# Performance work log

Hardware: AMD Instinct MI355X
Metric: run time of the kernel (lower is better)

## Reference

```python
import jax, jax.numpy as jnp
import numpy as np

B, N, D = 32, 2048, 128
HALF = D // 2
DT = 0.01  # interval = [0.0, 0.01], euler solver -> single step of size 0.01


def setup_inputs() -> dict:
    key = jax.random.key(0)
    ks = jax.random.split(key, 10)
    x = jax.random.normal(ks[0], (B, N, D), dtype=jnp.float32)
    hz = jax.random.normal(ks[1], (B, N, D), dtype=jnp.float32)
    # row-normalized random adjacency so adj @ h stays O(1) (avoids tanh saturation)
    adj = jax.random.uniform(ks[2], (N, N), dtype=jnp.float32) / N
    W1 = jax.random.normal(ks[3], (D, D), dtype=jnp.float32) * 0.05
    W2 = jax.random.normal(ks[4], (D, D), dtype=jnp.float32) * 0.05
    Wa = jax.random.normal(ks[5], (2 * D, 2 * D), dtype=jnp.float32) * 0.05
    ba = jnp.zeros((2 * D,), dtype=jnp.float32)
    Wb = jax.random.normal(ks[6], (2 * D, D), dtype=jnp.float32) * 0.05
    bb = jnp.zeros((D,), dtype=jnp.float32)
    # nn.Parameter init is zeros in torch; randomize in [0,0.1] for a nontrivial baseline
    eps = jax.random.uniform(ks[7], (B, N, HALF), dtype=jnp.float32) * 0.1
    return {"x": x, "hz": hz, "adj": adj, "W1": W1, "W2": W2,
            "Wa": Wa, "ba": ba, "Wb": Wb, "bb": bb, "eps": eps}


def reference(x, hz, adj, W1, W2, Wa, ba, Wb, bb, eps):
    # MLP gating: Linear(2D,2D) -> ReLU -> Linear(2D,D) -> Tanh
    u = jnp.concatenate([x, hz], axis=-1)            # [B,N,2D]
    h = jnp.tanh(jax.nn.relu(u @ Wa + ba) @ Wb + bb)  # [B,N,D]

    def gnn_func(h, W):
        # f(t, h) = tanh(A @ h @ W)  (graph diffusion ODE func)
        return jnp.tanh(jnp.einsum('nm,bmd->bnd', adj, h) @ W)

    def euler_step(h, W):
        # odeint(euler, t=[0, 0.01]): one step y1 = y0 + dt * f(0, y0)
        return h + DT * gnn_func(h, W)

    eps_c = jnp.clip(eps, 0.0, 0.1)
    for _ in range(2):
        h_f = euler_step(h, W1)[..., :HALF]                      # [B,N,D/2]
        h = jnp.concatenate([h_f, h[..., HALF:]], axis=-1)       # [B,N,D]
        h_s = eps_c * euler_step(h, W2)[..., HALF:]              # [B,N,D/2]
        h = jnp.concatenate([h_f, h_s], axis=-1)                 # [B,N,D]
    return h
```

## Files before the change

### kernel.cpp

```cpp
#include <hip/hip_runtime.h>


typedef unsigned short u16;
typedef unsigned char  u8;
typedef unsigned int   u32;
typedef unsigned long long u64;
typedef __attribute__((ext_vector_type(8))) short bf8;
typedef __attribute__((ext_vector_type(4))) float f4;

#define AS1 __attribute__((address_space(1)))
#define AS3 __attribute__((address_space(3)))

__device__ __forceinline__ void gl_lds16(const void* g, void* l) {
  __builtin_amdgcn_global_load_lds((const AS1 u32*)g, (AS3 u32*)l, 16, 0, 0);
}
__device__ __forceinline__ float bf2f(u16 v) {
  u32 u = ((u32)v) << 16; return __builtin_bit_cast(float, u);
}
__device__ __forceinline__ u16 f2bf(float f) {
  u32 u = __builtin_bit_cast(u32, f);
  return (u16)((u + 0x7fffu + ((u >> 16) & 1u)) >> 16);
}
__device__ __forceinline__ u8 f2fp8(float f) {
  u32 u = __builtin_bit_cast(u32, f);
  u32 s = (u >> 24) & 0x80u;
  int e = (int)((u >> 23) & 0xFFu) - 127;
  u32 m = u & 0x7FFFFFu;
  if (e > 8 || (e == 8 && m >= 0x700000u)) return (u8)(s | 0x7Eu);
  if (e >= -6) {
    u32 keep = m >> 20, rest = m & 0xFFFFFu;
    keep += (rest > 0x80000u || (rest == 0x80000u && (keep & 1u))) ? 1u : 0u;
    u32 v = ((u32)(e + 7) << 3) + keep;
    if (v >= 0x7Fu) v = 0x7Eu;
    return (u8)(s | v);
  }
  if (e < -10) return (u8)s;
  u32 mm = 0x800000u | m;
  int sh = 14 - e;
  u32 q = mm >> sh, rem = mm & ((1u << sh) - 1u), half = 1u << (sh - 1);
  q += (rem > half || (rem == half && (q & 1u))) ? 1u : 0u;
  return (u8)(s | q);
}
__device__ __forceinline__ float ldf(const void* p, size_t i, u32 isf32) {
  return isf32 ? ((const float*)p)[i] : bf2f(((const u16*)p)[i]);
}

__device__ __forceinline__ void stage128x32(const u16* grow0, int stride, u16* lds,
                                            int wave, int lane) {
  int r0 = wave * 16 + (lane >> 2);
  int c0 = (lane & 3) * 8;
  gl_lds16(grow0 + (size_t)r0 * stride + c0, lds + wave * 512);
  gl_lds16(grow0 + (size_t)(64 + r0) * stride + c0, lds + 2048 + wave * 512);
}

__global__ void detect_dtype(const u16* __restrict__ x_raw, u32* __restrict__ flag) {
  __shared__ int s;
  int tid = threadIdx.x;
  if (tid == 0) s = 0;
  __syncthreads();
  int huge = 0;
#pragma unroll
  for (int j = 0; j < 16; ++j) {
    u16 v = x_raw[tid * 16 + j];
    u32 e = (v >> 7) & 0xFF;
    if (e >= 0xC0) huge = 1;
  }
  if (huge) atomicOr(&s, 1);
  __syncthreads();
  if (tid == 0) flag[0] = (u32)s;
}

__global__ void cvt_fp8(const void* __restrict__ in, u8* __restrict__ out,
                        int n, const u32* __restrict__ flag) {
  u32 isf32 = flag[0];
  int gid = blockIdx.x * 256 + threadIdx.x;
  if (gid * 4 >= n) return;
  size_t i = (size_t)gid * 4;
  u32 pk = 0;
#pragma unroll
  for (int j = 0; j < 4; ++j)
    pk |= (u32)f2fp8(ldf(in, i + j, isf32) * 65536.0f) << (8 * j);
  *(u32*)&out[i] = pk;
}

__global__ void prep_weights(const void* __restrict__ Wa, const void* __restrict__ Wb,
                             const void* __restrict__ W1, const void* __restrict__ W2,
                             u16* __restrict__ WaT, u16* __restrict__ WbT,
                             u16* __restrict__ W1T, u16* __restrict__ W2T,
                             const u32* __restrict__ flag) {
  u32 isf32 = flag[0];
  int i = blockIdx.x * 256 + threadIdx.x;
  if (i < 65536) {
    int o = i >> 8, k = i & 255; WaT[o * 256 + k] = f2bf(ldf(Wa, (size_t)k * 256 + o, isf32));
  } else if (i < 98304) {
    int j = i - 65536; int o = j >> 8, k = j & 255;
    WbT[o * 256 + k] = f2bf(ldf(Wb, (size_t)k * 128 + o, isf32));
  } else if (i < 106496) {
    int j = i - 98304; int jj = j >> 7, k = j & 127;
    W1T[jj * 128 + k] = f2bf(ldf(W1, (size_t)k * 128 + jj, isf32));
  } else {
    int j = i - 106496; int jj = j >> 7, k = j & 127;
    W2T[jj * 128 + k] = f2bf(ldf(W2, (size_t)k * 128 + 64 + jj, isf32));
  }
}

__global__ __launch_bounds__(256, 2) void mlp_fused(const void* __restrict__ x,
                                                    const void* __restrict__ hz,
                                                    const u16* __restrict__ WaT,
                                                    const void* __restrict__ ba,
                                                    const u16* __restrict__ WbT,
                                                    const void* __restrict__ bb,
                                                    const u16* __restrict__ W1T,
                                                    u16* __restrict__ hT,
                                                    u8* __restrict__ hW,
                                                    const u32* __restrict__ flag) {
  __shared__ __align__(16) u16 Z[64 * 264];
  __shared__ __align__(16) u16 pool[10240];
  u16* lA = pool;
  u16* lB = pool + 2048;
  u16* hN = pool;
  u32 isf32 = flag[0];
  int tid = threadIdx.x, lane = tid & 63, wave = tid >> 6;
  int col = lane & 15, quad = lane >> 4;
  int r0 = blockIdx.x * 64;
  int b = r0 >> 11;

  f4 acc[4][4] = {};
  for (int kk = 0; kk < 8; ++kk) {
    int k0 = kk * 32;
    const void* src = (kk < 4) ? x : hz;
    int csrc = (kk < 4) ? k0 : (k0 - 128);
    __syncthreads();
    {
      int row = tid >> 2, c0 = (tid & 3) * 8;
      size_t g = (size_t)(r0 + row) * 128 + csrc + c0;
      uint4 pk;
      if (isf32) {
        f4 v0 = *(const f4*)&((const float*)src)[g];
        f4 v1 = *(const f4*)&((const float*)src)[g + 4];
        pk.x = (u32)f2bf(v0[0]) | ((u32)f2bf(v0[1]) << 16);
        pk.y = (u32)f2bf(v0[2]) | ((u32)f2bf(v0[3]) << 16);
        pk.z = (u32)f2bf(v1[0]) | ((u32)f2bf(v1[1]) << 16);
        pk.w = (u32)f2bf(v1[2]) | ((u32)f2bf(v1[3]) << 16);
      } else {
        pk = *(const uint4*)&((const u16*)src)[g];
      }
      *(uint4*)&lA[row * 32 + c0] = pk;
    }
    stage128x32(WaT + k0, 256, lB, wave, lane);
    stage128x32(WaT + (size_t)128 * 256 + k0, 256, lB + 4096, wave, lane);
    __syncthreads();
    bf8 af[4], bfr[4];
#pragma unroll
    for (int mi = 0; mi < 4; ++mi) af[mi] = *(const bf8*)&lA[(mi * 16 + col) * 32 + quad * 8];
#pragma unroll
    for (int nj = 0; nj < 4; ++nj) bfr[nj] = *(const bf8*)&lB[(wave * 64 + nj * 16 + col) * 32 + quad * 8];
#pragma unroll
    for (int mi = 0; mi < 4; ++mi)
#pragma unroll
      for (int nj = 0; nj < 4; ++nj)
        acc[mi][nj] = __builtin_amdgcn_mfma_f32_16x16x32_bf16(af[mi], bfr[nj], acc[mi][nj], 0, 0, 0);
  }
#pragma unroll
  for (int mi = 0; mi < 4; ++mi)
#pragma unroll
    for (int nj = 0; nj < 4; ++nj) {
      int o = wave * 64 + nj * 16 + col;
      float bav = ldf(ba, o, isf32);
      int rl = mi * 16 + quad * 4;
#pragma unroll
      for (int r = 0; r < 4; ++r)
        Z[(rl + r) * 264 + o] = f2bf(fmaxf(acc[mi][nj][r] + bav, 0.f));
    }
  __syncthreads();

  f4 acc2[4][2] = {};
  for (int kk = 0; kk < 8; ++kk) {
    int k0 = kk * 32;
    if (kk) __syncthreads();
    stage128x32(WbT + k0, 256, lB, wave, lane);
    __syncthreads();
    bf8 az[4], bw[2];
#pragma unroll
    for (int mi = 0; mi < 4; ++mi) az[mi] = *(const bf8*)&Z[(mi * 16 + col) * 264 + k0 + quad * 8];
#pragma unroll
    for (int nj = 0; nj < 2; ++nj) bw[nj] = *(const bf8*)&lB[(wave * 32 + nj * 16 + col) * 32 + quad * 8];
#pragma unroll
    for (int mi = 0; mi < 4; ++mi)
#pragma unroll
      for (int nj = 0; nj < 2; ++nj)
        acc2[mi][nj] = __builtin_amdgcn_mfma_f32_16x16x32_bf16(az[mi], bw[nj], acc2[mi][nj], 0, 0, 0);
  }
  __syncthreads();

#pragma unroll
  for (int mi = 0; mi < 4; ++mi)
#pragma unroll
    for (int nj = 0; nj < 2; ++nj) {
      int d = wave * 32 + nj * 16 + col;
      float bbv = ldf(bb, d, isf32);
      int rl = mi * 16 + quad * 4;
      int rabs = r0 + rl;
      int n = rabs & 2047;
      u16 p[4];
#pragma unroll
      for (int r = 0; r < 4; ++r) {
        p[r] = f2bf(tanhf(acc2[mi][nj][r] + bbv));
        hN[(rl + r) * 136 + d] = p[r];
      }
      u64 pk = (u64)p[0] | ((u64)p[1] << 16) | ((u64)p[2] << 32) | ((u64)p[3] << 48);
      *(u64*)&hT[(size_t)(b * 128 + d) * 2048 + n] = pk;
    }
  __syncthreads();

  f4 acc3[4] = {};
#pragma unroll
  for (int ks = 0; ks < 4; ++ks) {
    bf8 aw[4], bg;
#pragma unroll
    for (int mi = 0; mi < 4; ++mi)
      aw[mi] = *(const bf8*)&W1T[(size_t)(mi * 16 + col) * 128 + ks * 32 + quad * 8];
    bg = *(const bf8*)&hN[(wave * 16 + col) * 136 + ks * 32 + quad * 8];
#pragma unroll
    for (int mi = 0; mi < 4; ++mi)
      acc3[mi] = __builtin_amdgcn_mfma_f32_16x16x32_bf16(aw[mi], bg, acc3[mi], 0, 0, 0);
  }
#pragma unroll
  for (int mi = 0; mi < 4; ++mi) {
    int rloc = wave * 16 + col;
    int ng = (r0 & 2047) + rloc;
#pragma unroll
    for (int r = 0; r < 4; ++r) {
      int j = mi * 16 + quad * 4 + r;
      hW[(size_t)(b * 64 + j) * 2048 + ng] = f2fp8(acc3[mi][r]);
    }
  }
}

__global__ __launch_bounds__(256, 2) void fused_step2(const u16* __restrict__ hin,
                                                      const u8* __restrict__ hW8,
                                                      const u8* __restrict__ adj8,
                                                      const u16* __restrict__ WnT,
                                                      const void* __restrict__ eps,
                                                      u16* __restrict__ hout,
                                                      u8* __restrict__ hWout,
                                                      int half, const u32* __restrict__ flag) {
  __shared__ __align__(16) u16 smem[24576];
  u8* lA8 = (u8*)smem;
  u8* lB8 = lA8 + 16384;
  u16* gN = smem;
  u32 isf32 = flag[0];
  int tid = threadIdx.x, lane = tid & 63, wave = tid >> 6;
  int col = lane & 15, quad = lane >> 4;
  int b = blockIdx.y;
  int n0 = blockIdx.x * 128;

  const u8* Arow = hW8 + (size_t)(b * 64) * 2048;
  const u8* Brow = adj8 + (size_t)n0 * 2048;
  int r32 = lane & 31, kh16 = (lane >> 5) * 16;
  int baseQ = (quad >> 1) * 512 + (quad & 1) * 8 + col * 16;

  f4 acc[4][2] = {};
#pragma unroll 1
  for (int t = 0; t < 8; ++t) {
    {
      int ga = wave >> 1, kca0 = (wave & 1) * 4;
#pragma unroll
      for (int q = 0; q < 4; ++q) {
        int kc = kca0 + q;
        gl_lds16(Arow + (size_t)(ga * 32 + r32) * 2048 + t * 256 + kc * 32 + kh16,
                 lA8 + (ga * 8 + kc) * 1024);
      }
#pragma unroll
      for (int kc = 0; kc < 8; ++kc)
        gl_lds16(Brow + (size_t)(wave * 32 + r32) * 2048 + t * 256 + kc * 32 + kh16,
                 lB8 + (wave * 8 + kc) * 1024);
    }
    __syncthreads();
#pragma unroll
    for (int ks = 0; ks < 8; ++ks) {
      long long af[4], bfr[2];
#pragma unroll
      for (int mi = 0; mi < 4; ++mi)
        af[mi] = *(const long long*)&lA8[((mi >> 1) * 8 + ks) * 1024 + (mi & 1) * 256 + baseQ];
#pragma unroll
      for (int nj = 0; nj < 2; ++nj)
        bfr[nj] = *(const long long*)&lB8[(wave * 8 + ks) * 1024 + nj * 256 + baseQ];
#pragma unroll
      for (int mi = 0; mi < 4; ++mi)
#pragma unroll
        for (int nj = 0; nj < 2; ++nj)
          acc[mi][nj] = __builtin_amdgcn_mfma_f32_16x16x32_fp8_fp8(af[mi], bfr[nj], acc[mi][nj], 0, 0, 0);
    }
    __syncthreads();
  }

  bool has_eps = (eps != nullptr);
  bool mk_hw = (WnT != nullptr);
  int dBase = half * 64;
  const float INV = 1.52587890625e-05f;
#pragma unroll
  for (int mi = 0; mi < 4; ++mi)
#pragma unroll
    for (int nj = 0; nj < 2; ++nj) {
      int j0 = mi * 16 + quad * 4;
      int nl = wave * 32 + nj * 16 + col;
      int n = n0 + nl;
      float ev[4];
      if (has_eps) {
        size_t eoff = ((size_t)b * 2048 + n) * 64 + j0;
        if (isf32) {
          f4 e = *(const f4*)&((const float*)eps)[eoff];
          ev[0] = e[0]; ev[1] = e[1]; ev[2] = e[2]; ev[3] = e[3];
        } else {
          u64 e = *(const u64*)&((const u16*)eps)[eoff];
          ev[0] = bf2f((u16)e); ev[1] = bf2f((u16)(e >> 16));
          ev[2] = bf2f((u16)(e >> 32)); ev[3] = bf2f((u16)(e >> 48));
        }
      }
      u16 pv[4];
#pragma unroll
      for (int r = 0; r < 4; ++r) {
        int j = j0 + r;
        size_t idx = (size_t)(b * 128 + dBase + j) * 2048 + n;
        float hold = bf2f(hin[idx]);
        float nh = hold + 0.01f * tanhf(acc[mi][nj][r] * INV);
        if (has_eps) {
          float e = fminf(fmaxf(ev[r], 0.f), 0.1f);
          nh = e * nh;
        }
        pv[r] = f2bf(nh);
        hout[idx] = pv[r];
      }
      if (mk_hw) {
        u64 pk = (u64)pv[0] | ((u64)pv[1] << 16) | ((u64)pv[2] << 32) | ((u64)pv[3] << 48);
        *(u64*)&gN[nl * 136 + dBase + j0] = pk;
      }
    }

  {
    int oh = (1 - half) * 64;
    const u16* src = hin + (size_t)(b * 128 + oh) * 2048 + n0;
    u16* dst = hout + (size_t)(b * 128 + oh) * 2048 + n0;
#pragma unroll
    for (int i = 0; i < 4; ++i) {
      int idx = i * 256 + tid;
      int rr = idx >> 4;
      int cc = (idx & 15) * 8;
      uint4 v = *(const uint4*)&src[(size_t)rr * 2048 + cc];
      *(uint4*)&dst[(size_t)rr * 2048 + cc] = v;
      if (mk_hw) {
        u16 t[8];
        *(uint4*)t = v;
#pragma unroll
        for (int q = 0; q < 8; ++q) gN[(cc + q) * 136 + oh + rr] = t[q];
      }
    }
  }

  if (mk_hw) {
    __syncthreads();
    f4 acc2[4][2] = {};
#pragma unroll
    for (int ks = 0; ks < 4; ++ks) {
      bf8 aw[4], bg[2];
#pragma unroll
      for (int mi = 0; mi < 4; ++mi)
        aw[mi] = *(const bf8*)&WnT[(size_t)(mi * 16 + col) * 128 + ks * 32 + quad * 8];
#pragma unroll
      for (int nj = 0; nj < 2; ++nj)
        bg[nj] = *(const bf8*)&gN[(wave * 32 + nj * 16 + col) * 136 + ks * 32 + quad * 8];
#pragma unroll
      for (int mi = 0; mi < 4; ++mi)
#pragma unroll
        for (int nj = 0; nj < 2; ++nj)
          acc2[mi][nj] = __builtin_amdgcn_mfma_f32_16x16x32_bf16(aw[mi], bg[nj], acc2[mi][nj], 0, 0, 0);
    }
#pragma unroll
    for (int mi = 0; mi < 4; ++mi)
#pragma unroll
      for (int nj = 0; nj < 2; ++nj) {
        int jp0 = mi * 16 + quad * 4;
        int n = n0 + wave * 32 + nj * 16 + col;
#pragma unroll
        for (int r = 0; r < 4; ++r)
          hWout[(size_t)(b * 64 + jp0 + r) * 2048 + n] = f2fp8(acc2[mi][nj][r]);
      }
  }
}

__global__ void untranspose(const u16* __restrict__ hT, void* __restrict__ out,
                            const u32* __restrict__ flag) {
  __shared__ __align__(16) u16 t[64][65];
  u32 isf32 = flag[0];
  int b = blockIdx.z, d0 = blockIdx.y * 64, n0 = blockIdx.x * 64;
  int tid = threadIdx.x;
#pragma unroll
  for (int i = 0; i < 16; ++i) {
    int idx = tid + i * 256;
    int r = idx >> 6, c = idx & 63;
    t[r][c] = hT[(size_t)(b * 128 + d0 + r) * 2048 + n0 + c];
  }
  __syncthreads();
#pragma unroll
  for (int i = 0; i < 16; ++i) {
    int idx = tid + i * 256;
    int r = idx >> 6, c = idx & 63;
    size_t o = (size_t)(b * 2048 + n0 + r) * 128 + d0 + c;
    if (isf32) ((float*)out)[o] = bf2f(t[c][r]);
    else       ((u16*)out)[o] = t[c][r];
  }
}

extern "C" void kernel_launch(void* const* d_in, const int* in_sizes, int n_in,
                              void* d_out, int out_size, void* d_ws, size_t ws_size,
                              hipStream_t stream) {
  const void* x   = d_in[0];
  const void* hz  = d_in[1];
  const void* adj = d_in[2];
  const void* W1  = d_in[3];
  const void* W2  = d_in[4];
  const void* Wa  = d_in[5];
  const void* ba  = d_in[6];
  const void* Wb  = d_in[7];
  const void* bb  = d_in[8];
  const void* eps = d_in[9];

  char* ws = (char*)d_ws;
  u16* hA   = (u16*)(ws);
  u8*  adj8 = (u8*)(ws + (17ull << 20));
  u8*  hWa  = (u8*)(ws + (26ull << 20));
  u8*  hWb  = (u8*)(ws + (35ull << 20));
  u16* WaT  = (u16*)(ws + (44ull << 20));
  u16* WbT  = WaT + 256 * 256;
  u16* W1T  = WbT + 128 * 256;
  u16* W2T  = W1T + 64 * 128;
  u32* flag = (u32*)(W2T + 64 * 128);
  u16* hB   = (u16*)d_out;

  detect_dtype<<<dim3(1), dim3(256), 0, stream>>>((const u16*)x, flag);
  prep_weights<<<dim3(448), dim3(256), 0, stream>>>(Wa, Wb, W1, W2, WaT, WbT, W1T, W2T, flag);
  cvt_fp8<<<dim3(4096), dim3(256), 0, stream>>>(adj, adj8, 4194304, flag);
  mlp_fused<<<dim3(1024), dim3(256), 0, stream>>>(x, hz, WaT, ba, WbT, bb, W1T, hA, hWa, flag);
  fused_step2<<<dim3(16, 32), dim3(256), 0, stream>>>(hA, hWa, adj8, W2T, nullptr, hB, hWb, 0, flag);
  fused_step2<<<dim3(16, 32), dim3(256), 0, stream>>>(hB, hWb, adj8, W1T, eps, hA, hWa, 1, flag);
  fused_step2<<<dim3(16, 32), dim3(256), 0, stream>>>(hA, hWa, adj8, W2T, nullptr, hB, hWb, 0, flag);
  fused_step2<<<dim3(16, 32), dim3(256), 0, stream>>>(hB, hWb, adj8, nullptr, eps, hA, nullptr, 1, flag);
  untranspose<<<dim3(32, 2, 32), dim3(256), 0, stream>>>(hA, d_out, flag);
}
```

Baseline: 372.9 us.

## Read adjacency fragments directly from global memory and re-layout LDS staging tiles

```diff
diff --git a/kernel.cpp b/kernel.cpp
--- a/kernel.cpp
+++ b/kernel.cpp
@@ -45,12 +45,11 @@
   return isf32 ? ((const float*)p)[i] : bf2f(((const u16*)p)[i]);
 }
 
-__device__ __forceinline__ void stage128x32(const u16* grow0, int stride, u16* lds,
-                                            int wave, int lane) {
-  int r0 = wave * 16 + (lane >> 2);
-  int c0 = (lane & 3) * 8;
-  gl_lds16(grow0 + (size_t)r0 * stride + c0, lds + wave * 512);
-  gl_lds16(grow0 + (size_t)(64 + r0) * stride + c0, lds + 2048 + wave * 512);
+__device__ __forceinline__ void stage128x32q(const u16* g, int stride, u16* lds,
+                                             int wave, int lane) {
+  int r = lane & 15, qk = (lane >> 4) * 8;
+  gl_lds16(g + (size_t)(wave * 16 + r) * stride + qk, lds + wave * 512);
+  gl_lds16(g + (size_t)((wave + 4) * 16 + r) * stride + qk, lds + (wave + 4) * 512);
 }
 
 __global__ void detect_dtype(const u16* __restrict__ x_raw, u32* __restrict__ flag) {
@@ -145,16 +144,16 @@
       } else {
         pk = *(const uint4*)&((const u16*)src)[g];
       }
-      *(uint4*)&lA[row * 32 + c0] = pk;
-    }
-    stage128x32(WaT + k0, 256, lB, wave, lane);
-    stage128x32(WaT + (size_t)128 * 256 + k0, 256, lB + 4096, wave, lane);
+      *(uint4*)&lA[(row >> 4) * 512 + (tid & 3) * 128 + (row & 15) * 8] = pk;
+    }
+    stage128x32q(WaT + k0, 256, lB, wave, lane);
+    stage128x32q(WaT + (size_t)128 * 256 + k0, 256, lB + 4096, wave, lane);
     __syncthreads();
     bf8 af[4], bfr[4];
 #pragma unroll
-    for (int mi = 0; mi < 4; ++mi) af[mi] = *(const bf8*)&lA[(mi * 16 + col) * 32 + quad * 8];
-#pragma unroll
-    for (int nj = 0; nj < 4; ++nj) bfr[nj] = *(const bf8*)&lB[(wave * 64 + nj * 16 + col) * 32 + quad * 8];
+    for (int mi = 0; mi < 4; ++mi) af[mi] = *(const bf8*)&lA[mi * 512 + quad * 128 + col * 8];
+#pragma unroll
+    for (int nj = 0; nj < 4; ++nj) bfr[nj] = *(const bf8*)&lB[(wave * 4 + nj) * 512 + quad * 128 + col * 8];
 #pragma unroll
     for (int mi = 0; mi < 4; ++mi)
 #pragma unroll
@@ -178,13 +177,13 @@
   for (int kk = 0; kk < 8; ++kk) {
     int k0 = kk * 32;
     if (kk) __syncthreads();
-    stage128x32(WbT + k0, 256, lB, wave, lane);
+    stage128x32q(WbT + k0, 256, lB, wave, lane);
     __syncthreads();
     bf8 az[4], bw[2];
 #pragma unroll
     for (int mi = 0; mi < 4; ++mi) az[mi] = *(const bf8*)&Z[(mi * 16 + col) * 264 + k0 + quad * 8];
 #pragma unroll
-    for (int nj = 0; nj < 2; ++nj) bw[nj] = *(const bf8*)&lB[(wave * 32 + nj * 16 + col) * 32 + quad * 8];
+    for (int nj = 0; nj < 2; ++nj) bw[nj] = *(const bf8*)&lB[(wave * 2 + nj) * 512 + quad * 128 + col * 8];
 #pragma unroll
     for (int mi = 0; mi < 4; ++mi)
 #pragma unroll
@@ -245,9 +244,8 @@
                                                       u16* __restrict__ hout,
                                                       u8* __restrict__ hWout,
                                                       int half, const u32* __restrict__ flag) {
-  __shared__ __align__(16) u16 smem[24576];
+  __shared__ __align__(16) u16 smem[17408];
   u8* lA8 = (u8*)smem;
-  u8* lB8 = lA8 + 16384;
   u16* gN = smem;
   u32 isf32 = flag[0];
   int tid = threadIdx.x, lane = tid & 63, wave = tid >> 6;
@@ -256,36 +254,32 @@
   int n0 = blockIdx.x * 128;
 
   const u8* Arow = hW8 + (size_t)(b * 64) * 2048;
-  const u8* Brow = adj8 + (size_t)n0 * 2048;
+  const u8* Bb = adj8 + (size_t)(n0 + wave * 32 + col) * 2048 + quad * 8;
   int r32 = lane & 31, kh16 = (lane >> 5) * 16;
   int baseQ = (quad >> 1) * 512 + (quad & 1) * 8 + col * 16;
 
   f4 acc[4][2] = {};
 #pragma unroll 1
-  for (int t = 0; t < 8; ++t) {
+  for (int ch = 0; ch < 4; ++ch) {
     {
-      int ga = wave >> 1, kca0 = (wave & 1) * 4;
-#pragma unroll
-      for (int q = 0; q < 4; ++q) {
-        int kc = kca0 + q;
-        gl_lds16(Arow + (size_t)(ga * 32 + r32) * 2048 + t * 256 + kc * 32 + kh16,
-                 lA8 + (ga * 8 + kc) * 1024);
-      }
-#pragma unroll
-      for (int kc = 0; kc < 8; ++kc)
-        gl_lds16(Brow + (size_t)(wave * 32 + r32) * 2048 + t * 256 + kc * 32 + kh16,
-                 lB8 + (wave * 8 + kc) * 1024);
-    }
-    __syncthreads();
-#pragma unroll
-    for (int ks = 0; ks < 8; ++ks) {
-      long long af[4], bfr[2];
+      int g = wave >> 1, kc0 = (wave & 1) * 8;
+      const u8* As = Arow + (size_t)(g * 32 + r32) * 2048 + ch * 512 + kh16;
+      u8* Ad = lA8 + g * 16384 + kc0 * 1024;
+#pragma unroll
+      for (int q = 0; q < 8; ++q)
+        gl_lds16(As + (kc0 + q) * 32, Ad + q * 1024);
+    }
+    __syncthreads();
+#pragma unroll
+    for (int ks = 0; ks < 16; ++ks) {
+      long long bfr[2];
+#pragma unroll
+      for (int nj = 0; nj < 2; ++nj)
+        bfr[nj] = *(const long long*)&Bb[(size_t)nj * 16 * 2048 + ch * 512 + ks * 32];
+      long long af[4];
 #pragma unroll
       for (int mi = 0; mi < 4; ++mi)
-        af[mi] = *(const long long*)&lA8[((mi >> 1) * 8 + ks) * 1024 + (mi & 1) * 256 + baseQ];
-#pragma unroll
-      for (int nj = 0; nj < 2; ++nj)
-        bfr[nj] = *(const long long*)&lB8[(wave * 8 + ks) * 1024 + nj * 256 + baseQ];
+        af[mi] = *(const long long*)&lA8[((mi >> 1) * 16 + ks) * 1024 + (mi & 1) * 256 + baseQ];
 #pragma unroll
       for (int mi = 0; mi < 4; ++mi)
 #pragma unroll
```

Result: slower. 437.0 us (+17.2%).

## Halve fused_step2 node tile to 64, raise occupancy, swizzle block order

Applied to the files above, without the earlier changes.

```diff
diff --git a/kernel.cpp b/kernel.cpp
--- a/kernel.cpp
+++ b/kernel.cpp
@@ -237,7 +237,7 @@
   }
 }
 
-__global__ __launch_bounds__(256, 2) void fused_step2(const u16* __restrict__ hin,
+__global__ __launch_bounds__(256, 4) void fused_step2(const u16* __restrict__ hin,
                                                       const u8* __restrict__ hW8,
                                                       const u8* __restrict__ adj8,
                                                       const u16* __restrict__ WnT,
@@ -245,52 +245,50 @@
                                                       u16* __restrict__ hout,
                                                       u8* __restrict__ hWout,
                                                       int half, const u32* __restrict__ flag) {
-  __shared__ __align__(16) u16 smem[24576];
+  __shared__ __align__(16) u16 smem[16384];
   u8* lA8 = (u8*)smem;
   u8* lB8 = lA8 + 16384;
   u16* gN = smem;
   u32 isf32 = flag[0];
   int tid = threadIdx.x, lane = tid & 63, wave = tid >> 6;
   int col = lane & 15, quad = lane >> 4;
-  int b = blockIdx.y;
-  int n0 = blockIdx.x * 128;
+
+  int bid = blockIdx.y * 32 + blockIdx.x;
+  int sw = (bid & 7) * 128 + (bid >> 3);
+  int b = sw >> 5;
+  int n0 = (sw & 31) * 64;
 
   const u8* Arow = hW8 + (size_t)(b * 64) * 2048;
   const u8* Brow = adj8 + (size_t)n0 * 2048;
   int r32 = lane & 31, kh16 = (lane >> 5) * 16;
   int baseQ = (quad >> 1) * 512 + (quad & 1) * 8 + col * 16;
 
-  f4 acc[4][2] = {};
+  f4 acc[4] = {};
 #pragma unroll 1
-  for (int t = 0; t < 8; ++t) {
+  for (int ch = 0; ch < 8; ++ch) {
     {
-      int ga = wave >> 1, kca0 = (wave & 1) * 4;
+      int g = wave >> 1, kc0 = (wave & 1) * 4;
+      const u8* As = Arow + (size_t)(g * 32 + r32) * 2048 + ch * 256 + kh16;
+      const u8* Bs = Brow + (size_t)(g * 32 + r32) * 2048 + ch * 256 + kh16;
+      u8* Ad = lA8 + g * 8192 + kc0 * 1024;
+      u8* Bd = lB8 + g * 8192 + kc0 * 1024;
 #pragma unroll
       for (int q = 0; q < 4; ++q) {
-        int kc = kca0 + q;
-        gl_lds16(Arow + (size_t)(ga * 32 + r32) * 2048 + t * 256 + kc * 32 + kh16,
-                 lA8 + (ga * 8 + kc) * 1024);
-      }
-#pragma unroll
-      for (int kc = 0; kc < 8; ++kc)
-        gl_lds16(Brow + (size_t)(wave * 32 + r32) * 2048 + t * 256 + kc * 32 + kh16,
-                 lB8 + (wave * 8 + kc) * 1024);
+        gl_lds16(As + (kc0 + q) * 32, Ad + q * 1024);
+        gl_lds16(Bs + (kc0 + q) * 32, Bd + q * 1024);
+      }
     }
     __syncthreads();
 #pragma unroll
     for (int ks = 0; ks < 8; ++ks) {
-      long long af[4], bfr[2];
+      long long af[4], bfr;
+      bfr = *(const long long*)&lB8[(wave >> 1) * 8192 + ks * 1024 + (wave & 1) * 256 + baseQ];
 #pragma unroll
       for (int mi = 0; mi < 4; ++mi)
-        af[mi] = *(const long long*)&lA8[((mi >> 1) * 8 + ks) * 1024 + (mi & 1) * 256 + baseQ];
-#pragma unroll
-      for (int nj = 0; nj < 2; ++nj)
-        bfr[nj] = *(const long long*)&lB8[(wave * 8 + ks) * 1024 + nj * 256 + baseQ];
+        af[mi] = *(const long long*)&lA8[(mi >> 1) * 8192 + ks * 1024 + (mi & 1) * 256 + baseQ];
 #pragma unroll
       for (int mi = 0; mi < 4; ++mi)
-#pragma unroll
-        for (int nj = 0; nj < 2; ++nj)
-          acc[mi][nj] = __builtin_amdgcn_mfma_f32_16x16x32_fp8_fp8(af[mi], bfr[nj], acc[mi][nj], 0, 0, 0);
+        acc[mi] = __builtin_amdgcn_mfma_f32_16x16x32_fp8_fp8(af[mi], bfr, acc[mi], 0, 0, 0);
     }
     __syncthreads();
   }
@@ -299,54 +297,52 @@
   bool mk_hw = (WnT != nullptr);
   int dBase = half * 64;
   const float INV = 1.52587890625e-05f;
-#pragma unroll
-  for (int mi = 0; mi < 4; ++mi)
-#pragma unroll
-    for (int nj = 0; nj < 2; ++nj) {
-      int j0 = mi * 16 + quad * 4;
-      int nl = wave * 32 + nj * 16 + col;
-      int n = n0 + nl;
-      float ev[4];
+  int nl = wave * 16 + col;
+  int n = n0 + nl;
+#pragma unroll
+  for (int mi = 0; mi < 4; ++mi) {
+    int j0 = mi * 16 + quad * 4;
+    float ev[4];
+    if (has_eps) {
+      size_t eoff = ((size_t)b * 2048 + n) * 64 + j0;
+      if (isf32) {
+        f4 e = *(const f4*)&((const float*)eps)[eoff];
+        ev[0] = e[0]; ev[1] = e[1]; ev[2] = e[2]; ev[3] = e[3];
+      } else {
+        u64 e = *(const u64*)&((const u16*)eps)[eoff];
+        ev[0] = bf2f((u16)e); ev[1] = bf2f((u16)(e >> 16));
+        ev[2] = bf2f((u16)(e >> 32)); ev[3] = bf2f((u16)(e >> 48));
+      }
+    }
+    u16 pv[4];
+#pragma unroll
+    for (int r = 0; r < 4; ++r) {
+      int j = j0 + r;
+      size_t idx = (size_t)(b * 128 + dBase + j) * 2048 + n;
+      float hold = bf2f(hin[idx]);
+      float nh = hold + 0.01f * tanhf(acc[mi][r] * INV);
       if (has_eps) {
-        size_t eoff = ((size_t)b * 2048 + n) * 64 + j0;
-        if (isf32) {
-          f4 e = *(const f4*)&((const float*)eps)[eoff];
-          ev[0] = e[0]; ev[1] = e[1]; ev[2] = e[2]; ev[3] = e[3];
-        } else {
-          u64 e = *(const u64*)&((const u16*)eps)[eoff];
-          ev[0] = bf2f((u16)e); ev[1] = bf2f((u16)(e >> 16));
-          ev[2] = bf2f((u16)(e >> 32)); ev[3] = bf2f((u16)(e >> 48));
-        }
-      }
-      u16 pv[4];
-#pragma unroll
-      for (int r = 0; r < 4; ++r) {
-        int j = j0 + r;
-        size_t idx = (size_t)(b * 128 + dBase + j) * 2048 + n;
-        float hold = bf2f(hin[idx]);
-        float nh = hold + 0.01f * tanhf(acc[mi][nj][r] * INV);
-        if (has_eps) {
-          float e = fminf(fmaxf(ev[r], 0.f), 0.1f);
-          nh = e * nh;
-        }
-        pv[r] = f2bf(nh);
-        hout[idx] = pv[r];
-      }
-      if (mk_hw) {
-        u64 pk = (u64)pv[0] | ((u64)pv[1] << 16) | ((u64)pv[2] << 32) | ((u64)pv[3] << 48);
-        *(u64*)&gN[nl * 136 + dBase + j0] = pk;
-      }
-    }
+        float e = fminf(fmaxf(ev[r], 0.f), 0.1f);
+        nh = e * nh;
+      }
+      pv[r] = f2bf(nh);
+      hout[idx] = pv[r];
+    }
+    if (mk_hw) {
+      u64 pk = (u64)pv[0] | ((u64)pv[1] << 16) | ((u64)pv[2] << 32) | ((u64)pv[3] << 48);
+      *(u64*)&gN[nl * 136 + dBase + j0] = pk;
+    }
+  }
 
   {
     int oh = (1 - half) * 64;
     const u16* src = hin + (size_t)(b * 128 + oh) * 2048 + n0;
     u16* dst = hout + (size_t)(b * 128 + oh) * 2048 + n0;
 #pragma unroll
-    for (int i = 0; i < 4; ++i) {
+    for (int i = 0; i < 2; ++i) {
       int idx = i * 256 + tid;
-      int rr = idx >> 4;
-      int cc = (idx & 15) * 8;
+      int rr = idx >> 3;
+      int cc = (idx & 7) * 8;
       uint4 v = *(const uint4*)&src[(size_t)rr * 2048 + cc];
       *(uint4*)&dst[(size_t)rr * 2048 + cc] = v;
       if (mk_hw) {
@@ -360,32 +356,26 @@
 
   if (mk_hw) {
     __syncthreads();
-    f4 acc2[4][2] = {};
+    f4 acc2[4] = {};
 #pragma unroll
     for (int ks = 0; ks < 4; ++ks) {
-      bf8 aw[4], bg[2];
+      bf8 aw[4], bg;
 #pragma unroll
       for (int mi = 0; mi < 4; ++mi)
         aw[mi] = *(const bf8*)&WnT[(size_t)(mi * 16 + col) * 128 + ks * 32 + quad * 8];
-#pragma unroll
-      for (int nj = 0; nj < 2; ++nj)
-        bg[nj] = *(const bf8*)&gN[(wave * 32 + nj * 16 + col) * 136 + ks * 32 + quad * 8];
+      bg = *(const bf8*)&gN[(wave * 16 + col) * 136 + ks * 32 + quad * 8];
 #pragma unroll
       for (int mi = 0; mi < 4; ++mi)
-#pragma unroll
-        for (int nj = 0; nj < 2; ++nj)
-          acc2[mi][nj] = __builtin_amdgcn_mfma_f32_16x16x32_bf16(aw[mi], bg[nj], acc2[mi][nj], 0, 0, 0);
-    }
-#pragma unroll
-    for (int mi = 0; mi < 4; ++mi)
-#pragma unroll
-      for (int nj = 0; nj < 2; ++nj) {
-        int jp0 = mi * 16 + quad * 4;
-        int n = n0 + wave * 32 + nj * 16 + col;
-#pragma unroll
-        for (int r = 0; r < 4; ++r)
-          hWout[(size_t)(b * 64 + jp0 + r) * 2048 + n] = f2fp8(acc2[mi][nj][r]);
-      }
+        acc2[mi] = __builtin_amdgcn_mfma_f32_16x16x32_bf16(aw[mi], bg, acc2[mi], 0, 0, 0);
+    }
+#pragma unroll
+    for (int mi = 0; mi < 4; ++mi) {
+      int jp0 = mi * 16 + quad * 4;
+      int ng = n0 + wave * 16 + col;
+#pragma unroll
+      for (int r = 0; r < 4; ++r)
+        hWout[(size_t)(b * 64 + jp0 + r) * 2048 + ng] = f2fp8(acc2[mi][r]);
+    }
   }
 }
 
@@ -442,9 +432,9 @@
   prep_weights<<<dim3(448), dim3(256), 0, stream>>>(Wa, Wb, W1, W2, WaT, WbT, W1T, W2T, flag);
   cvt_fp8<<<dim3(4096), dim3(256), 0, stream>>>(adj, adj8, 4194304, flag);
   mlp_fused<<<dim3(1024), dim3(256), 0, stream>>>(x, hz, WaT, ba, WbT, bb, W1T, hA, hWa, flag);
-  fused_step2<<<dim3(16, 32), dim3(256), 0, stream>>>(hA, hWa, adj8, W2T, nullptr, hB, hWb, 0, flag);
-  fused_step2<<<dim3(16, 32), dim3(256), 0, stream>>>(hB, hWb, adj8, W1T, eps, hA, hWa, 1, flag);
-  fused_step2<<<dim3(16, 32), dim3(256), 0, stream>>>(hA, hWa, adj8, W2T, nullptr, hB, hWb, 0, flag);
-  fused_step2<<<dim3(16, 32), dim3(256), 0, stream>>>(hB, hWb, adj8, nullptr, eps, hA, nullptr, 1, flag);
+  fused_step2<<<dim3(32, 32), dim3(256), 0, stream>>>(hA, hWa, adj8, W2T, nullptr, hB, hWb, 0, flag);
+  fused_step2<<<dim3(32, 32), dim3(256), 0, stream>>>(hB, hWb, adj8, W1T, eps, hA, hWa, 1, flag);
+  fused_step2<<<dim3(32, 32), dim3(256), 0, stream>>>(hA, hWa, adj8, W2T, nullptr, hB, hWb, 0, flag);
+  fused_step2<<<dim3(32, 32), dim3(256), 0, stream>>>(hB, hWb, adj8, nullptr, eps, hA, nullptr, 1, flag);
   untranspose<<<dim3(32, 2, 32), dim3(256), 0, stream>>>(hA, d_out, flag);
 }
```

Result: slower. 410.3 us (+10.0%).
